# Kernel optimization log

Measured on AMD Instinct MI355X. Metric: run time of the kernel, lower is better.

Reference implementation:

```python
import jax, jax.numpy as jnp
import numpy as np

EPS = 1e-5  # torch LayerNorm default


def _layer_norm(x, w, b):
    # normalized_shape = [C, K, K] -> normalize over last 3 dims
    m = jnp.mean(x, axis=(-3, -2, -1), keepdims=True)
    v = jnp.var(x, axis=(-3, -2, -1), keepdims=True)
    return (x - m) * jax.lax.rsqrt(v + EPS) * w + b


def setup_inputs() -> dict:
    key = jax.random.key(0)
    k0, k1, k2, k3, k4, k5 = jax.random.split(key, 6)
    B, C, H, W, K = 32, 192, 56, 56, 7
    x = jax.random.normal(k0, (B, C, H, W), jnp.float32)
    ln0_w = jax.random.normal(k1, (C, K, K), jnp.float32)
    ln0_b = jax.random.normal(k2, (C, K, K), jnp.float32)
    conv0_w = jax.random.normal(k3, (C, 1, K, K), jnp.float32) * 0.1
    ln1_w = jax.random.normal(k4, (C, K, K), jnp.float32)
    ln1_b = jax.random.normal(k5, (C, K, K), jnp.float32)
    return {"x": x, "ln0_w": ln0_w, "ln0_b": ln0_b, "conv0_w": conv0_w,
            "ln1_w": ln1_w, "ln1_b": ln1_b}


def reference(x, ln0_w, ln0_b, conv0_w, ln1_w, ln1_b):
    B, C, H, W = x.shape
    K = conv0_w.shape[-1]
    # AdaptiveAvgPool2d((K,K)); H,W divisible by K -> uniform average pooling
    p = x.reshape(B, C, K, H // K, K, W // K).mean(axis=(3, 5))  # [B,C,K,K]
    p = _layer_norm(p, ln0_w, ln0_b)
    # depthwise KxK conv on KxK map, padding 'same'
    p = jax.lax.conv_general_dilated(
        p, conv0_w, window_strides=(1, 1), padding='SAME',
        dimension_numbers=('NCHW', 'OIHW', 'NCHW'), feature_group_count=C)
    p = jax.nn.relu(_layer_norm(p, ln1_w, ln1_b))  # [B,C,K,K] dynamic kernels
    # per-sample, per-channel depthwise conv: fold batch into channels
    ker = p.reshape(B * C, 1, K, K)
    out = jax.lax.conv_general_dilated(
        x.reshape(1, B * C, H, W), ker, window_strides=(1, 1), padding='SAME',
        dimension_numbers=('NCHW', 'OIHW', 'NCHW'), feature_group_count=B * C)
    return out.reshape(B, C, H, W)
```

## Files before the change

### kernel.cpp

```cpp
#include <hip/hip_runtime.h>

#define BB 32
#define CC 192
#define HH 56
#define WW 56
#define KS 7
#define HW 3136
#define KK 49
#define CKK 9408
#define PL 8
#define NCELL (BB * CC * KK)
#define NBC (BB * CC)
#define P0BLK 37
#define MIDBLK 24
#define TABW 56

typedef _Float16 h2 __attribute__((ext_vector_type(2)));

__device__ __forceinline__ unsigned int pack16(float a, float b) {
    return __builtin_bit_cast(unsigned int, __builtin_amdgcn_cvt_pkrtz(a, b));
}

__global__ __launch_bounds__(256) void pool_kernel(const float* __restrict__ x,
                                                   float* __restrict__ p0,
                                                   float2* __restrict__ part0) {
    __shared__ float red[8];
    int b = blockIdx.x / P0BLK;
    int t = blockIdx.x - b * P0BLK;
    int cell = t * 256 + threadIdx.x;
    float v = 0.f;
    if (cell < CKK) {
        int c = cell / KK;
        int r = cell - c * KK;
        int i = r / KS;
        int j = r - i * KS;
        const float* src = x + ((size_t)(b * CC + c)) * HW + (i * PL) * WW + j * PL;
        float s = 0.f;
#pragma unroll
        for (int a = 0; a < PL; ++a) {
            float4 v0 = *(const float4*)(src + a * WW);
            float4 v1 = *(const float4*)(src + a * WW + 4);
            s += v0.x + v0.y + v0.z + v0.w + v1.x + v1.y + v1.z + v1.w;
        }
        v = s * (1.f / 64.f);
        p0[b * CKK + cell] = v;
    }
    float sv = v, sq = v * v;
#pragma unroll
    for (int o = 32; o > 0; o >>= 1) {
        sv += __shfl_down(sv, o, 64);
        sq += __shfl_down(sq, o, 64);
    }
    if ((threadIdx.x & 63) == 0) {
        red[(threadIdx.x >> 6) * 2 + 0] = sv;
        red[(threadIdx.x >> 6) * 2 + 1] = sq;
    }
    __syncthreads();
    if (threadIdx.x == 0)
        part0[blockIdx.x] = make_float2(red[0] + red[2] + red[4] + red[6],
                                        red[1] + red[3] + red[5] + red[7]);
}

__global__ __launch_bounds__(512) void mid_kernel(
    const float* __restrict__ p0,
    const float* __restrict__ ln0w, const float* __restrict__ ln0b,
    const float* __restrict__ w0,
    const float2* __restrict__ part0,
    float* __restrict__ q1,
    float2* __restrict__ part1)
{
    __shared__ float red[16];
    int tid  = threadIdx.x;
    int lane = tid & 63;
    int bc   = blockIdx.x * 8 + (tid >> 6);
    int b = bc / CC;
    int c = bc - b * CC;

    float s0 = 0.f, ss0 = 0.f;
    if (lane < P0BLK) {
        float2 p = part0[b * P0BLK + lane];
        s0 = p.x; ss0 = p.y;
    }
#pragma unroll
    for (int o = 32; o > 0; o >>= 1) {
        s0  += __shfl_down(s0, o, 64);
        ss0 += __shfl_down(ss0, o, 64);
    }
    s0  = __shfl(s0, 0, 64);
    ss0 = __shfl(ss0, 0, 64);
    float mean = s0 * (1.f / CKK);
    float rstd = rsqrtf(ss0 * (1.f / CKK) - mean * mean + 1e-5f);

    float val = 0.f;
    if (lane < KK)
        val = (p0[bc * KK + lane] - mean) * rstd * ln0w[c * KK + lane]
              + ln0b[c * KK + lane];

    int i0 = lane / KS;
    int j0 = lane - i0 * KS;
    const float* wc = w0 + c * KK;

    float acc = 0.f;
#pragma unroll
    for (int u = 0; u < KS; ++u) {
        int ii = i0 + u - 3;
#pragma unroll
        for (int v = 0; v < KS; ++v) {
            int jj = j0 + v - 3;
            bool ok = (ii >= 0) && (ii < KS) && (jj >= 0) && (jj < KS);
            int sl = ok ? (ii * KS + jj) : 0;
            float sv = __shfl(val, sl, 64);
            acc += ok ? sv * wc[u * KS + v] : 0.f;
        }
    }
    if (lane >= KK) acc = 0.f;
    if (lane < KK) q1[bc * KK + lane] = acc;

    float s2 = acc, ss2 = acc * acc;
#pragma unroll
    for (int o = 32; o > 0; o >>= 1) {
        s2  += __shfl_down(s2, o, 64);
        ss2 += __shfl_down(ss2, o, 64);
    }
    if (lane == 0) {
        red[(tid >> 6) * 2 + 0] = s2;
        red[(tid >> 6) * 2 + 1] = ss2;
    }
    __syncthreads();
    if (tid == 0) {
        float a = 0.f, q = 0.f;
#pragma unroll
        for (int w = 0; w < 8; ++w) { a += red[2 * w]; q += red[2 * w + 1]; }
        part1[blockIdx.x] = make_float2(a, q);
    }
}

__global__ __launch_bounds__(256) void tab_kernel(
    const float* __restrict__ q1, const float2* __restrict__ part1,
    const float* __restrict__ ln1w, const float* __restrict__ ln1b,
    unsigned int* __restrict__ ktab)
{
    int lane = threadIdx.x & 63;
    int bc   = blockIdx.x * 4 + (threadIdx.x >> 6);
    int b = bc / CC;
    int c = bc - b * CC;

    float s1 = 0.f, ss1 = 0.f;
    if (lane < MIDBLK) {
        float2 p = part1[b * MIDBLK + lane];
        s1 = p.x; ss1 = p.y;
    }
#pragma unroll
    for (int o = 32; o > 0; o >>= 1) {
        s1  += __shfl_down(s1, o, 64);
        ss1 += __shfl_down(ss1, o, 64);
    }
    s1  = __shfl(s1, 0, 64);
    ss1 = __shfl(ss1, 0, 64);
    float m = s1 * (1.f / CKK);
    float r = rsqrtf(ss1 * (1.f / CKK) - m * m + 1e-5f);

    float kt = 0.f;
    if (lane < KK) {
        float v = (q1[(size_t)bc * KK + lane] - m) * r * ln1w[c * KK + lane]
                  + ln1b[c * KK + lane];
        kt = v > 0.f ? v : 0.f;
    }

    bool isDt = lane < 28;
    int idx = isDt ? lane : (lane < TABW ? lane - 28 : 0);
    int d = idx / KS, v = idx - KS * d;
    int i0 = 2 * d * KS + v;
    int ip = i0 + KS > 48 ? 48 : i0 + KS;
    int im = i0 - KS < 0  ? 0  : i0 - KS;
    float vi0 = __shfl(kt, i0, 64);
    float vip = __shfl(kt, ip, 64);
    float vim = __shfl(kt, im, 64);
    float a = isDt ? vi0 : (d > 0 ? vim : 0.f);
    float bb = isDt ? (d < 3 ? vip : 0.f) : vi0;
    unsigned int w = pack16(a, bb);
    if (lane < TABW)
        ktab[(size_t)bc * TABW + lane] = w;
}

__global__ __launch_bounds__(256) void conv_kernel(
    const float* __restrict__ x,
    const unsigned int* __restrict__ ktab,
    float* __restrict__ out)
{
    __shared__ unsigned int tile[32 * 64];
    int bc   = blockIdx.x;
    int tid  = threadIdx.x;
    int lane = tid & 63;
    int wid  = tid >> 6;

    const uint4* tb = (const uint4*)(ktab + (size_t)bc * TABW);
    unsigned int dt[28], ct[28];
#pragma unroll
    for (int i = 0; i < 7; ++i) {
        uint4 t4 = tb[i];
        dt[4 * i + 0] = t4.x; dt[4 * i + 1] = t4.y;
        dt[4 * i + 2] = t4.z; dt[4 * i + 3] = t4.w;
    }
#pragma unroll
    for (int i = 0; i < 7; ++i) {
        uint4 t4 = tb[7 + i];
        ct[4 * i + 0] = t4.x; ct[4 * i + 1] = t4.y;
        ct[4 * i + 2] = t4.z; ct[4 * i + 3] = t4.w;
    }

    const float* src = x + (size_t)bc * HW;
    int t0 = tid, t1 = tid + 256;
    int pr2a = 1 + t0 / 14, qa = t0 - (pr2a - 1) * 14;
    int pr2b = 1 + t1 / 14, qb = t1 - (pr2b - 1) * 14;
    bool has1 = t1 < 29 * 14;
    int rAa = 2 * pr2a - 3, rBa = rAa + 1;
    int rAb = 2 * pr2b - 3, rBb = rAb + 1;
    float4 z4 = make_float4(0.f, 0.f, 0.f, 0.f);
    float4 a0 = (rAa >= 0) ? *(const float4*)(src + rAa * WW + 4 * qa) : z4;
    float4 b0 = *(const float4*)(src + rBa * WW + 4 * qa);
    float4 a1 = z4, b1 = z4;
    if (has1) {
        a1 = *(const float4*)(src + rAb * WW + 4 * qb);
        b1 = (rBb < HH) ? *(const float4*)(src + rBb * WW + 4 * qb) : z4;
    }

    if (tid < 232) {
        int pr2 = 1 + (tid >> 3);
        int j = tid & 7;
        tile[pr2 * 64 + (j < 4 ? j : 56 + j)] = 0u;
    }
    if (tid >= 224) {
        int i = tid - 224;
        int pr2 = (i < 16) ? 0 : 30;
        *(uint4*)(tile + pr2 * 64 + 4 * (i & 15)) = make_uint4(0, 0, 0, 0);
    }

    {
        *(uint4*)(tile + pr2a * 64 + 4 + 4 * qa) =
            make_uint4(pack16(a0.x, b0.x), pack16(a0.y, b0.y),
                       pack16(a0.z, b0.z), pack16(a0.w, b0.w));
    }
    if (has1) {
        *(uint4*)(tile + pr2b * 64 + 4 + 4 * qb) =
            make_uint4(pack16(a1.x, b1.x), pack16(a1.y, b1.y),
                       pack16(a1.z, b1.z), pack16(a1.w, b1.w));
    }
    __syncthreads();

    int r0 = wid * 14;
    const unsigned int* base = tile + (wid * 7) * 64 + lane + 1;
    float accL[7], accH[7];
#pragma unroll
    for (int t = 0; t < 7; ++t) { accL[t] = 0.f; accH[t] = 0.f; }

    unsigned int wa[KS], wb[KS];
#pragma unroll
    for (int j = 0; j < KS; ++j) wa[j] = base[j];

#define H2(u) __builtin_bit_cast(h2, (u))
#define CONV_STEP(S, CUR)                                                     \
    {                                                                         \
        _Pragma("unroll")                                                     \
        for (int d = 0; d < 4; ++d) {                                         \
            int t = (S) - d;                                                  \
            if (t >= 0 && t <= 6) {                                           \
                _Pragma("unroll")                                             \
                for (int vv = 0; vv < KS; ++vv) {                             \
                    accL[t] = __builtin_amdgcn_fdot2(H2(CUR[vv]),             \
                                  H2(dt[d * KS + vv]), accL[t], false);       \
                    accH[t] = __builtin_amdgcn_fdot2(H2(CUR[vv]),             \
                                  H2(ct[d * KS + vv]), accH[t], false);       \
                }                                                             \
            }                                                                 \
        }                                                                     \
    }

#pragma unroll
    for (int ss = 0; ss < 5; ++ss) {
        int s0 = 2 * ss, s1 = 2 * ss + 1;
        {
            const unsigned int* np = base + s1 * 64;
#pragma unroll
            for (int j = 0; j < KS; ++j) wb[j] = np[j];
        }
        CONV_STEP(s0, wa);
        if (ss < 4) {
            const unsigned int* np = base + (s0 + 2) * 64;
#pragma unroll
            for (int j = 0; j < KS; ++j) wa[j] = np[j];
        }
        CONV_STEP(s1, wb);
    }
#undef CONV_STEP
#undef H2

    if (lane < WW) {
        float* ob = out + (size_t)bc * HW + r0 * WW + lane;
#pragma unroll
        for (int t = 0; t < 7; ++t) {
            ob[(2 * t) * WW]     = accL[t];
            ob[(2 * t + 1) * WW] = accH[t];
        }
    }
}

extern "C" void kernel_launch(void* const* d_in, const int* in_sizes, int n_in,
                              void* d_out, int out_size, void* d_ws, size_t ws_size,
                              hipStream_t stream) {
    const float* x    = (const float*)d_in[0];
    const float* ln0w = (const float*)d_in[1];
    const float* ln0b = (const float*)d_in[2];
    const float* w0   = (const float*)d_in[3];
    const float* ln1w = (const float*)d_in[4];
    const float* ln1b = (const float*)d_in[5];
    float* out = (float*)d_out;

    float*  p0    = (float*)d_ws;
    float*  q1    = p0 + NCELL;
    float2* part0 = (float2*)(q1 + NCELL);
    float2* part1 = part0 + BB * P0BLK;
    unsigned int* ktab = (unsigned int*)(part1 + BB * MIDBLK);

    pool_kernel<<<BB * P0BLK, 256, 0, stream>>>(x, p0, part0);
    mid_kernel <<<BB * MIDBLK, 512, 0, stream>>>(p0, ln0w, ln0b, w0, part0, q1, part1);
    tab_kernel <<<NBC / 4, 256, 0, stream>>>(q1, part1, ln1w, ln1b, ktab);
    conv_kernel<<<NBC, 256, 0, stream>>>(x, ktab, out);
}
```

Before: 59.29 us.

## Emit packed fp16 padded input from pool kernel and read it directly in conv

The pool kernel, which already reads all of x, now also writes a padded, row-pair-packed fp16 copy of each channel plane to workspace. The conv kernel reads that packed buffer straight from global memory, dropping its fp32 load, LDS staging, pack step and block barrier. The row-pair alignment changes from odd/even to even/odd, so the kernel table and the accumulation schedule are remapped and an extra step is added. The cost is an extra workspace write and read of half the size of x, and conv operand loads now come from global memory or cache instead of LDS.

```diff
diff --git a/kernel.cpp b/kernel.cpp
--- a/kernel.cpp
+++ b/kernel.cpp
@@ -14,6 +14,7 @@
 #define P0BLK 37
 #define MIDBLK 24
 #define TABW 56
+#define XP 2048
 
 typedef _Float16 h2 __attribute__((ext_vector_type(2)));
 
@@ -23,7 +24,8 @@
 
 __global__ __launch_bounds__(256) void pool_kernel(const float* __restrict__ x,
                                                    float* __restrict__ p0,
-                                                   float2* __restrict__ part0) {
+                                                   float2* __restrict__ part0,
+                                                   unsigned int* __restrict__ x16) {
     __shared__ float red[8];
     int b = blockIdx.x / P0BLK;
     int t = blockIdx.x - b * P0BLK;
@@ -34,16 +36,54 @@
         int r = cell - c * KK;
         int i = r / KS;
         int j = r - i * KS;
-        const float* src = x + ((size_t)(b * CC + c)) * HW + (i * PL) * WW + j * PL;
+        int bc = b * CC + c;
+        const float* src = x + (size_t)bc * HW + (i * PL) * WW + j * PL;
+        unsigned int* xp = x16 + (size_t)bc * XP;
+        uint4 z = make_uint4(0u, 0u, 0u, 0u);
         float s = 0.f;
 #pragma unroll
-        for (int a = 0; a < PL; ++a) {
-            float4 v0 = *(const float4*)(src + a * WW);
-            float4 v1 = *(const float4*)(src + a * WW + 4);
-            s += v0.x + v0.y + v0.z + v0.w + v1.x + v1.y + v1.z + v1.w;
+        for (int p = 0; p < 4; ++p) {
+            float4 aA = *(const float4*)(src + (2 * p) * WW);
+            float4 aB = *(const float4*)(src + (2 * p) * WW + 4);
+            float4 bA = *(const float4*)(src + (2 * p + 1) * WW);
+            float4 bB = *(const float4*)(src + (2 * p + 1) * WW + 4);
+            s += aA.x + aA.y + aA.z + aA.w + aB.x + aB.y + aB.z + aB.w
+               + bA.x + bA.y + bA.z + bA.w + bB.x + bB.y + bB.z + bB.w;
+            int pr2 = 4 * i + p + 2;
+            *(uint4*)(xp + pr2 * 64 + 4 + 8 * j) =
+                make_uint4(pack16(aA.x, bA.x), pack16(aA.y, bA.y),
+                           pack16(aA.z, bA.z), pack16(aA.w, bA.w));
+            *(uint4*)(xp + pr2 * 64 + 8 + 8 * j) =
+                make_uint4(pack16(aB.x, bB.x), pack16(aB.y, bB.y),
+                           pack16(aB.z, bB.z), pack16(aB.w, bB.w));
         }
         v = s * (1.f / 64.f);
         p0[b * CKK + cell] = v;
+
+        if (i == 0) {
+            *(uint4*)(xp + 0 * 64 + 4 + 8 * j) = z;
+            *(uint4*)(xp + 0 * 64 + 8 + 8 * j) = z;
+            *(uint4*)(xp + 1 * 64 + 4 + 8 * j) = z;
+            *(uint4*)(xp + 1 * 64 + 8 + 8 * j) = z;
+        }
+        if (i == 6) {
+            *(uint4*)(xp + 30 * 64 + 4 + 8 * j) = z;
+            *(uint4*)(xp + 30 * 64 + 8 + 8 * j) = z;
+            *(uint4*)(xp + 31 * 64 + 4 + 8 * j) = z;
+            *(uint4*)(xp + 31 * 64 + 8 + 8 * j) = z;
+        }
+        if (j == 0) {
+#pragma unroll
+            for (int p = 0; p < 4; ++p) *(uint4*)(xp + (4 * i + p + 2) * 64) = z;
+            if (i == 0) { *(uint4*)(xp + 0) = z;        *(uint4*)(xp + 64) = z; }
+            if (i == 6) { *(uint4*)(xp + 30 * 64) = z;  *(uint4*)(xp + 31 * 64) = z; }
+        }
+        if (j == 6) {
+#pragma unroll
+            for (int p = 0; p < 4; ++p) *(uint4*)(xp + (4 * i + p + 2) * 64 + 60) = z;
+            if (i == 0) { *(uint4*)(xp + 60) = z;           *(uint4*)(xp + 64 + 60) = z; }
+            if (i == 6) { *(uint4*)(xp + 30 * 64 + 60) = z; *(uint4*)(xp + 31 * 64 + 60) = z; }
+        }
     }
     float sv = v, sq = v * v;
 #pragma unroll
@@ -169,26 +209,24 @@
 
     bool isDt = lane < 28;
     int idx = isDt ? lane : (lane < TABW ? lane - 28 : 0);
-    int d = idx / KS, v = idx - KS * d;
-    int i0 = 2 * d * KS + v;
-    int ip = i0 + KS > 48 ? 48 : i0 + KS;
-    int im = i0 - KS < 0  ? 0  : i0 - KS;
-    float vi0 = __shfl(kt, i0, 64);
-    float vip = __shfl(kt, ip, 64);
-    float vim = __shfl(kt, im, 64);
-    float a = isDt ? vi0 : (d > 0 ? vim : 0.f);
-    float bb = isDt ? (d < 3 ? vip : 0.f) : vi0;
-    unsigned int w = pack16(a, bb);
+    int e = idx / KS, v = idx - KS * e;
+    int iA, iB; bool mA, mB;
+    if (isDt) { mA = (e > 0); iA = mA ? (2 * e - 1) * KS + v : 0;
+                mB = true;    iB = 2 * e * KS + v; }
+    else      { mA = true;    iA = 2 * e * KS + v;
+                mB = (e < 3); iB = mB ? (2 * e + 1) * KS + v : 0; }
+    float va = __shfl(kt, iA, 64);
+    float vb = __shfl(kt, iB, 64);
+    unsigned int w = pack16(mA ? va : 0.f, mB ? vb : 0.f);
     if (lane < TABW)
         ktab[(size_t)bc * TABW + lane] = w;
 }
 
 __global__ __launch_bounds__(256) void conv_kernel(
-    const float* __restrict__ x,
+    const unsigned int* __restrict__ x16,
     const unsigned int* __restrict__ ktab,
     float* __restrict__ out)
 {
-    __shared__ unsigned int tile[32 * 64];
     int bc   = blockIdx.x;
     int tid  = threadIdx.x;
     int lane = tid & 63;
@@ -209,47 +247,9 @@
         ct[4 * i + 2] = t4.z; ct[4 * i + 3] = t4.w;
     }
 
-    const float* src = x + (size_t)bc * HW;
-    int t0 = tid, t1 = tid + 256;
-    int pr2a = 1 + t0 / 14, qa = t0 - (pr2a - 1) * 14;
-    int pr2b = 1 + t1 / 14, qb = t1 - (pr2b - 1) * 14;
-    bool has1 = t1 < 29 * 14;
-    int rAa = 2 * pr2a - 3, rBa = rAa + 1;
-    int rAb = 2 * pr2b - 3, rBb = rAb + 1;
-    float4 z4 = make_float4(0.f, 0.f, 0.f, 0.f);
-    float4 a0 = (rAa >= 0) ? *(const float4*)(src + rAa * WW + 4 * qa) : z4;
-    float4 b0 = *(const float4*)(src + rBa * WW + 4 * qa);
-    float4 a1 = z4, b1 = z4;
-    if (has1) {
-        a1 = *(const float4*)(src + rAb * WW + 4 * qb);
-        b1 = (rBb < HH) ? *(const float4*)(src + rBb * WW + 4 * qb) : z4;
-    }
-
-    if (tid < 232) {
-        int pr2 = 1 + (tid >> 3);
-        int j = tid & 7;
-        tile[pr2 * 64 + (j < 4 ? j : 56 + j)] = 0u;
-    }
-    if (tid >= 224) {
-        int i = tid - 224;
-        int pr2 = (i < 16) ? 0 : 30;
-        *(uint4*)(tile + pr2 * 64 + 4 * (i & 15)) = make_uint4(0, 0, 0, 0);
-    }
-
-    {
-        *(uint4*)(tile + pr2a * 64 + 4 + 4 * qa) =
-            make_uint4(pack16(a0.x, b0.x), pack16(a0.y, b0.y),
-                       pack16(a0.z, b0.z), pack16(a0.w, b0.w));
-    }
-    if (has1) {
-        *(uint4*)(tile + pr2b * 64 + 4 + 4 * qb) =
-            make_uint4(pack16(a1.x, b1.x), pack16(a1.y, b1.y),
-                       pack16(a1.z, b1.z), pack16(a1.w, b1.w));
-    }
-    __syncthreads();
-
-    int r0 = wid * 14;
-    const unsigned int* base = tile + (wid * 7) * 64 + lane + 1;
+    int ll = lane < 56 ? lane : 55;
+    const unsigned int* base = x16 + (size_t)bc * XP + (wid * 7) * 64 + ll + 1;
+
     float accL[7], accH[7];
 #pragma unroll
     for (int t = 0; t < 7; ++t) { accL[t] = 0.f; accH[t] = 0.f; }
@@ -262,16 +262,20 @@
 #define CONV_STEP(S, CUR)                                                     \
     {                                                                         \
         _Pragma("unroll")                                                     \
-        for (int d = 0; d < 4; ++d) {                                         \
-            int t = (S) - d;                                                  \
-            if (t >= 0 && t <= 6) {                                           \
+        for (int e = 0; e < 4; ++e) {                                         \
+            int tl = (S) - e;                                                 \
+            if (tl >= 0 && tl <= 6) {                                         \
                 _Pragma("unroll")                                             \
-                for (int vv = 0; vv < KS; ++vv) {                             \
-                    accL[t] = __builtin_amdgcn_fdot2(H2(CUR[vv]),             \
-                                  H2(dt[d * KS + vv]), accL[t], false);       \
-                    accH[t] = __builtin_amdgcn_fdot2(H2(CUR[vv]),             \
-                                  H2(ct[d * KS + vv]), accH[t], false);       \
-                }                                                             \
+                for (int vv = 0; vv < KS; ++vv)                               \
+                    accL[tl] = __builtin_amdgcn_fdot2(H2(CUR[vv]),            \
+                                   H2(dt[e * KS + vv]), accL[tl], false);     \
+            }                                                                 \
+            int th = (S) - 1 - e;                                             \
+            if (th >= 0 && th <= 6) {                                         \
+                _Pragma("unroll")                                             \
+                for (int vv = 0; vv < KS; ++vv)                               \
+                    accH[th] = __builtin_amdgcn_fdot2(H2(CUR[vv]),            \
+                                   H2(ct[e * KS + vv]), accH[th], false);     \
             }                                                                 \
         }                                                                     \
     }
@@ -285,18 +289,19 @@
             for (int j = 0; j < KS; ++j) wb[j] = np[j];
         }
         CONV_STEP(s0, wa);
-        if (ss < 4) {
+        {
             const unsigned int* np = base + (s0 + 2) * 64;
 #pragma unroll
             for (int j = 0; j < KS; ++j) wa[j] = np[j];
         }
         CONV_STEP(s1, wb);
     }
+    CONV_STEP(10, wa);
 #undef CONV_STEP
 #undef H2
 
     if (lane < WW) {
-        float* ob = out + (size_t)bc * HW + r0 * WW + lane;
+        float* ob = out + (size_t)bc * HW + (wid * 14) * WW + lane;
 #pragma unroll
         for (int t = 0; t < 7; ++t) {
             ob[(2 * t) * WW]     = accL[t];
@@ -321,9 +326,10 @@
     float2* part0 = (float2*)(q1 + NCELL);
     float2* part1 = part0 + BB * P0BLK;
     unsigned int* ktab = (unsigned int*)(part1 + BB * MIDBLK);
-
-    pool_kernel<<<BB * P0BLK, 256, 0, stream>>>(x, p0, part0);
+    unsigned int* x16  = ktab + (size_t)NBC * TABW;
+
+    pool_kernel<<<BB * P0BLK, 256, 0, stream>>>(x, p0, part0, x16);
     mid_kernel <<<BB * MIDBLK, 512, 0, stream>>>(p0, ln0w, ln0b, w0, part0, q1, part1);
     tab_kernel <<<NBC / 4, 256, 0, stream>>>(q1, part1, ln1w, ln1b, ktab);
-    conv_kernel<<<NBC, 256, 0, stream>>>(x, ktab, out);
-}
+    conv_kernel<<<NBC, 256, 0, stream>>>(x16, ktab, out);
+}
```

Measured after the change: 66.73 us. +12.5%, slower.
